# Kernel optimization log

Measured on AMD Instinct MI355X. Metric: run time of the kernel, lower is better.

## Reference

```python
import jax, jax.numpy as jnp
import numpy as np

N_HEAD = 16
N_QUERY_GROUPS = 4
HEAD_SIZE = 64
ROPE_THETA = 10000.0


def apply_rope(x, theta=ROPE_THETA):
    # x: (B, H, T, D) -- lucidrains interleaved-pair rotary embedding
    B, H, T, D = x.shape
    inv_freq = 1.0 / (theta ** (jnp.arange(0, D, 2, dtype=jnp.float32) / D))  # (D/2,)
    freqs = jnp.arange(T, dtype=jnp.float32)[:, None] * inv_freq[None, :]      # (T, D/2)
    freqs = jnp.repeat(freqs, 2, axis=-1)                                      # (T, D)
    cos = jnp.cos(freqs).astype(x.dtype)
    sin = jnp.sin(freqs).astype(x.dtype)
    x1 = x[..., 0::2]
    x2 = x[..., 1::2]
    rot = jnp.stack((-x2, x1), axis=-1).reshape(x.shape)  # rotate_half, interleaved
    return x * cos + rot * sin


def setup_inputs() -> dict:
    key = jax.random.key(0)
    k1, k2, k3 = jax.random.split(key, 3)
    n_embd = N_HEAD * HEAD_SIZE
    qkv_dim = (N_HEAD + 2 * N_QUERY_GROUPS) * HEAD_SIZE
    x = jax.random.normal(k1, (1, 2048, n_embd), dtype=jnp.float32)
    w_attn = jax.random.normal(k2, (n_embd, qkv_dim), dtype=jnp.float32) * (n_embd ** -0.5)
    w_proj = jax.random.normal(k3, (n_embd, n_embd), dtype=jnp.float32) * (n_embd ** -0.5)
    return {"x": x, "w_attn": w_attn, "w_proj": w_proj}


def reference(x, w_attn, w_proj):
    B, T, C = x.shape
    q_per_kv = N_HEAD // N_QUERY_GROUPS
    total_qkv = q_per_kv + 2
    qkv = (x @ w_attn).reshape(B, T, N_QUERY_GROUPS, total_qkv, HEAD_SIZE)
    q = qkv[:, :, :, :q_per_kv, :].reshape(B, T, N_HEAD, HEAD_SIZE)
    k = qkv[:, :, :, q_per_kv:q_per_kv + 1, :].reshape(B, T, N_QUERY_GROUPS, HEAD_SIZE)
    v = qkv[:, :, :, q_per_kv + 1:, :].reshape(B, T, N_QUERY_GROUPS, HEAD_SIZE)
    # (B, H, T, D)
    q = q.transpose(0, 2, 1, 3)
    k = k.transpose(0, 2, 1, 3)
    v = v.transpose(0, 2, 1, 3)
    q = apply_rope(q)
    k = apply_rope(k)
    # GQA: broadcast each kv group to its q_per_kv query heads (repeat_interleave)
    k = jnp.repeat(k, q_per_kv, axis=1)
    v = jnp.repeat(v, q_per_kv, axis=1)
    scale = 1.0 / jnp.sqrt(jnp.asarray(HEAD_SIZE, dtype=q.dtype))
    att = jnp.einsum('bhqd,bhkd->bhqk', q, k) * scale
    causal = jnp.tril(jnp.ones((T, T), dtype=bool))
    att = jnp.where(causal, att, jnp.asarray(-jnp.inf, dtype=att.dtype))
    att = jax.nn.softmax(att, axis=-1)
    y = jnp.einsum('bhqk,bhkd->bhqd', att, v)
    y = y.transpose(0, 2, 1, 3).reshape(B, T, N_HEAD * HEAD_SIZE)
    return y @ w_proj
```

## Files before the change

kernel.cpp:

```cpp
#include <hip/hip_runtime.h>

#define T_SEQ 2048
#define C_EMB 1024
#define C_QKV 1536
#define N_HEAD 16

typedef __bf16 bf16x8 __attribute__((ext_vector_type(8)));
typedef __bf16 bf16x4 __attribute__((ext_vector_type(4)));
typedef float  f32x4  __attribute__((ext_vector_type(4)));

__device__ __forceinline__ void load_lds16(const __bf16* g, __bf16* l)
{
    __builtin_amdgcn_global_load_lds(
        (const __attribute__((address_space(1))) unsigned int*)g,
        (__attribute__((address_space(3))) unsigned int*)l, 16, 0, 0);
}

__device__ __forceinline__ void tconv_tile(
    const float* __restrict__ in, __bf16* __restrict__ out,
    int R, int C, int r0, int c0, float (*lds)[65], int t)
{
#pragma unroll
    for (int k = 0; k < 16; k++) {
        int r = k * 4 + (t >> 6), c = t & 63;
        lds[r][c] = in[(size_t)(r0 + r) * C + c0 + c];
    }
    __syncthreads();
#pragma unroll
    for (int k = 0; k < 16; k++) {
        int cc = k * 4 + (t >> 6), rr = t & 63;
        out[(size_t)(c0 + cc) * R + r0 + rr] = (__bf16)lds[rr][cc];
    }
}

__global__ __launch_bounds__(256) void prep_kernel(
    const float* __restrict__ x, const float* __restrict__ wa,
    const float* __restrict__ wp, __bf16* __restrict__ x_bf,
    __bf16* __restrict__ waT, __bf16* __restrict__ wpT)
{
    __shared__ float lds[64][65];
    const int b = blockIdx.x, t = threadIdx.x;
    if (b < 384) {
        tconv_tile(wa, waT, C_EMB, C_QKV, (b / 24) * 64, (b % 24) * 64, lds, t);
    } else if (b < 640) {
        int b2 = b - 384;
        tconv_tile(wp, wpT, C_EMB, C_EMB, (b2 / 16) * 64, (b2 % 16) * 64, lds, t);
    } else {
        for (int gi = (b - 640) * 256 + t; gi < T_SEQ * C_EMB / 8; gi += 65536) {
            float4 v0 = ((const float4*)x)[gi * 2];
            float4 v1 = ((const float4*)x)[gi * 2 + 1];
            bf16x8 o = { (__bf16)v0.x, (__bf16)v0.y, (__bf16)v0.z, (__bf16)v0.w,
                         (__bf16)v1.x, (__bf16)v1.y, (__bf16)v1.z, (__bf16)v1.w };
            ((bf16x8*)x_bf)[gi] = o;
        }
    }
}

template <bool FUSE_QKV>
__global__ __launch_bounds__(256) void gemm_mfma_kernel(
    const __bf16* __restrict__ A, const __bf16* __restrict__ Bt,
    __bf16* __restrict__ Cq, __bf16* __restrict__ Vt,
    float* __restrict__ Cf, int M, int N, int K)
{
    __shared__ __align__(16) __bf16 As0[64 * 64], As1[64 * 64];
    __shared__ __align__(16) __bf16 Bs0[64 * 64], Bs1[64 * 64];

    const int tid = threadIdx.x;
    const int l = tid & 63, w = tid >> 6;
    const int ln = l & 15, q = l >> 4;
    const int wm = (w & 1) * 32, wn = (w >> 1) * 32;
    const int row0 = blockIdx.y * 64, col0 = blockIdx.x * 64;

    f32x4 acc[2][2];
#pragma unroll
    for (int mi = 0; mi < 2; mi++)
#pragma unroll
        for (int ni = 0; ni < 2; ni++) acc[mi][ni] = (f32x4){0.f, 0.f, 0.f, 0.f};

    auto stage = [&](int k0, __bf16* as, __bf16* bs) {
#pragma unroll
        for (int p = 0; p < 2; p++) {
            int r = p * 32 + w * 8 + (l >> 3);
            int cc = (l & 7) ^ (r & 7);
            load_lds16(A + (size_t)(row0 + r) * K + k0 + cc * 8,
                       as + p * 2048 + w * 512);
            load_lds16(Bt + (size_t)(col0 + r) * K + k0 + cc * 8,
                       bs + p * 2048 + w * 512);
        }
    };
    auto compute = [&](const __bf16* as, const __bf16* bs) {
#pragma unroll
        for (int ki = 0; ki < 2; ki++) {
            bf16x8 af[2], bfr[2];
#pragma unroll
            for (int mi = 0; mi < 2; mi++)
                af[mi] = *(const bf16x8*)&as[(wm + mi * 16 + ln) * 64 +
                                             (((ki * 4 + q) ^ (ln & 7)) * 8)];
#pragma unroll
            for (int ni = 0; ni < 2; ni++)
                bfr[ni] = *(const bf16x8*)&bs[(wn + ni * 16 + ln) * 64 +
                                              (((ki * 4 + q) ^ (ln & 7)) * 8)];
#pragma unroll
            for (int mi = 0; mi < 2; mi++)
#pragma unroll
                for (int ni = 0; ni < 2; ni++)
                    acc[mi][ni] = __builtin_amdgcn_mfma_f32_16x16x32_bf16(
                        af[mi], bfr[ni], acc[mi][ni], 0, 0, 0);
        }
    };

    stage(0, As0, Bs0);
    for (int k0 = 0;; k0 += 128) {
        __syncthreads();
        if (k0 + 64 < K) stage(k0 + 64, As1, Bs1);
        compute(As0, Bs0);
        if (k0 + 64 >= K) break;
        __syncthreads();
        if (k0 + 128 < K) stage(k0 + 128, As0, Bs0);
        compute(As1, Bs1);
        if (k0 + 128 >= K) break;
    }

#pragma unroll
    for (int mi = 0; mi < 2; mi++)
#pragma unroll
        for (int ni = 0; ni < 2; ni++) {
            const int col = col0 + wn + ni * 16 + ln;
            if (!FUSE_QKV) {
#pragma unroll
                for (int reg = 0; reg < 4; reg++) {
                    int row = row0 + wm + mi * 16 + 4 * q + reg;
                    Cf[(size_t)row * N + col] = acc[mi][ni][reg];
                }
            } else {
                const int r = col % 384;
                const int gg = col / 384;
                if (r < 320) {
                    const int d = r & 63;
                    const float inv_freq =
                        __expf(-(float)(d & ~1) * (9.210340371976184f / 64.0f));
                    const float sgn = (d & 1) ? 1.0f : -1.0f;
                    const float osc = (r < 256) ? 0.18033688011112042f : 1.0f;
#pragma unroll
                    for (int reg = 0; reg < 4; reg++) {
                        int row = row0 + wm + mi * 16 + 4 * q + reg;
                        float v = acc[mi][ni][reg];
                        float pv = __shfl_xor(v, 1, 64);
                        float sn, cs;
                        sincosf((float)row * inv_freq, &sn, &cs);
                        Cq[(size_t)row * C_QKV + col] =
                            (__bf16)((v * cs + sgn * pv * sn) * osc);
                    }
                } else {
                    const int d = r - 320;
#pragma unroll
                    for (int reg = 0; reg < 4; reg++) {
                        int row = row0 + wm + mi * 16 + 4 * q + reg;
                        Vt[(size_t)(gg * 64 + d) * T_SEQ + row] =
                            (__bf16)acc[mi][ni][reg];
                    }
                }
            }
        }
}

__global__ __launch_bounds__(256) void attn_mfma_kernel(
    const __bf16* __restrict__ qkv, const __bf16* __restrict__ Vt,
    __bf16* __restrict__ y)
{
    __shared__ __align__(16) __bf16 Ks0[64 * 64], Ks1[64 * 64];
    __shared__ __align__(16) __bf16 Vs0[64 * 64], Vs1[64 * 64];
    __shared__ __align__(16) __bf16 Ps[64 * 72];

    const int tid = threadIdx.x;
    const int l = tid & 63, w = tid >> 6;
    const int ln = l & 15, q = l >> 4;
    const int h = blockIdx.y;
    const int qb = (h & 8) ? (31 - blockIdx.x) : blockIdx.x;
    const int g = h >> 2, hj = h & 3;
    const int qbase = g * 384 + hj * 64;
    const int kbase = g * 384 + 256;

    const int qrow = qb * 64 + w * 16 + ln;
    bf16x8 qa[2];
#pragma unroll
    for (int ki = 0; ki < 2; ki++)
        qa[ki] = *(const bf16x8*)(qkv + (size_t)qrow * C_QKV + qbase +
                                  ki * 32 + q * 8);

    f32x4 O[4];
#pragma unroll
    for (int ni = 0; ni < 4; ni++) O[ni] = (f32x4){0.f, 0.f, 0.f, 0.f};
    float lsum = 0.f;

    auto stage = [&](int kt, __bf16* ks, __bf16* vs) {
#pragma unroll
        for (int p = 0; p < 2; p++) {
            int r = p * 32 + w * 8 + (l >> 3);
            int cc = (l & 7) ^ (r & 7);
            load_lds16(qkv + (size_t)(kt * 64 + r) * C_QKV + kbase + cc * 8,
                       ks + p * 2048 + w * 512);
            load_lds16(Vt + (size_t)(g * 64 + r) * T_SEQ + kt * 64 + cc * 8,
                       vs + p * 2048 + w * 512);
        }
    };
    auto compute = [&](int kt, const __bf16* ks, const __bf16* vs) {
        f32x4 s[4];
#pragma unroll
        for (int ni = 0; ni < 4; ni++) s[ni] = (f32x4){0.f, 0.f, 0.f, 0.f};
#pragma unroll
        for (int ki = 0; ki < 2; ki++)
#pragma unroll
            for (int ni = 0; ni < 4; ni++) {
                bf16x8 kb = *(const bf16x8*)&ks[(ni * 16 + ln) * 64 +
                                                (((ki * 4 + q) ^ (ln & 7)) * 8)];
                s[ni] = __builtin_amdgcn_mfma_f32_16x16x32_bf16(
                    kb, qa[ki], s[ni], 0, 0, 0);
            }

        const bool diag = (kt == qb);
#pragma unroll
        for (int ni = 0; ni < 4; ni++) {
            bf16x4 pp;
#pragma unroll
            for (int reg = 0; reg < 4; reg++) {
                float v = s[ni][reg];
                if (diag && (ni * 16 + 4 * q + reg) > (w * 16 + ln)) v = -1e30f;
                float p = exp2f(v);
                lsum += p;
                pp[reg] = (__bf16)p;
            }
            *(bf16x4*)&Ps[(w * 16 + ln) * 72 + ni * 16 + 4 * q] = pp;
        }

#pragma unroll
        for (int ki = 0; ki < 2; ki++) {
            bf16x8 pa = *(const bf16x8*)&Ps[(w * 16 + ln) * 72 +
                                            ki * 32 + q * 8];
#pragma unroll
            for (int ni = 0; ni < 4; ni++) {
                bf16x8 vb = *(const bf16x8*)&vs[(ni * 16 + ln) * 64 +
                                                (((ki * 4 + q) ^ (ln & 7)) * 8)];
                O[ni] = __builtin_amdgcn_mfma_f32_16x16x32_bf16(
                    vb, pa, O[ni], 0, 0, 0);
            }
        }
    };

    stage(0, Ks0, Vs0);
    for (int kt = 0;; kt += 2) {
        __syncthreads();
        if (kt + 1 <= qb) stage(kt + 1, Ks1, Vs1);
        compute(kt, Ks0, Vs0);
        if (kt + 1 > qb) break;
        __syncthreads();
        if (kt + 2 <= qb) stage(kt + 2, Ks0, Vs0);
        compute(kt + 1, Ks1, Vs1);
        if (kt + 2 > qb) break;
    }

    float ls = lsum;
    ls += __shfl_xor(ls, 16, 64);
    ls += __shfl_xor(ls, 32, 64);
    const float inv = 1.0f / ls;
    const int t = qb * 64 + w * 16 + ln;
#pragma unroll
    for (int ni = 0; ni < 4; ni++) {
        bf16x4 o;
#pragma unroll
        for (int reg = 0; reg < 4; reg++) o[reg] = (__bf16)(O[ni][reg] * inv);
        *(bf16x4*)&y[(size_t)t * C_EMB + h * 64 + ni * 16 + 4 * q] = o;
    }
}

extern "C" void kernel_launch(void* const* d_in, const int* in_sizes, int n_in,
                              void* d_out, int out_size, void* d_ws, size_t ws_size,
                              hipStream_t stream)
{
    const float* x      = (const float*)d_in[0];
    const float* w_attn = (const float*)d_in[1];
    const float* w_proj = (const float*)d_in[2];
    float* out = (float*)d_out;

    __bf16* x_bf = (__bf16*)d_ws;
    __bf16* waT  = x_bf + (size_t)T_SEQ * C_EMB;
    __bf16* wpT  = waT  + (size_t)C_QKV * C_EMB;
    __bf16* qkv  = wpT  + (size_t)C_EMB * C_EMB;
    __bf16* Vt   = qkv  + (size_t)T_SEQ * C_QKV;
    __bf16* y_bf = Vt   + (size_t)256 * T_SEQ;

    prep_kernel<<<896, 256, 0, stream>>>(x, w_attn, w_proj, x_bf, waT, wpT);

    gemm_mfma_kernel<true><<<dim3(C_QKV / 64, T_SEQ / 64), 256, 0, stream>>>(
        x_bf, waT, qkv, Vt, nullptr, T_SEQ, C_QKV, C_EMB);

    attn_mfma_kernel<<<dim3(32, N_HEAD), 256, 0, stream>>>(qkv, Vt, y_bf);

    gemm_mfma_kernel<false><<<dim3(C_EMB / 64, T_SEQ / 64), 256, 0, stream>>>(
        y_bf, wpT, nullptr, nullptr, out, T_SEQ, C_EMB, C_EMB);
}
```

Before: 122.9 us.

## Split long causal attention rows across two blocks and merge partial results

```diff
diff --git a/kernel.cpp b/kernel.cpp
--- a/kernel.cpp
+++ b/kernel.cpp
@@ -166,7 +166,8 @@
 
 __global__ __launch_bounds__(256) void attn_mfma_kernel(
     const __bf16* __restrict__ qkv, const __bf16* __restrict__ Vt,
-    __bf16* __restrict__ y)
+    __bf16* __restrict__ y, __bf16* __restrict__ Opart,
+    float* __restrict__ lpart)
 {
     __shared__ __align__(16) __bf16 Ks0[64 * 64], Ks1[64 * 64];
     __shared__ __align__(16) __bf16 Vs0[64 * 64], Vs1[64 * 64];
@@ -175,8 +176,13 @@
     const int tid = threadIdx.x;
     const int l = tid & 63, w = tid >> 6;
     const int ln = l & 15, q = l >> 4;
-    const int h = blockIdx.y;
-    const int qb = (h & 8) ? (31 - blockIdx.x) : blockIdx.x;
+    const int x = blockIdx.x, h = blockIdx.y;
+    int qb, t0, t1;
+    bool partial;
+    if (x < 16)      { qb = 15 - x;  t0 = 0;             t1 = qb + 1;        partial = false; }
+    else if (x < 32) { qb = x;       t0 = 0;             t1 = (qb + 2) >> 1; partial = true;  }
+    else             { qb = x - 16;  t0 = (qb + 2) >> 1; t1 = qb + 1;        partial = true;  }
+
     const int g = h >> 2, hj = h & 3;
     const int qbase = g * 384 + hj * 64;
     const int kbase = g * 384 + 256;
@@ -247,30 +253,65 @@
         }
     };
 
-    stage(0, Ks0, Vs0);
-    for (int kt = 0;; kt += 2) {
+    stage(t0, Ks0, Vs0);
+    for (int kt = t0;;) {
         __syncthreads();
-        if (kt + 1 <= qb) stage(kt + 1, Ks1, Vs1);
+        if (kt + 1 < t1) stage(kt + 1, Ks1, Vs1);
         compute(kt, Ks0, Vs0);
-        if (kt + 1 > qb) break;
+        if (++kt >= t1) break;
         __syncthreads();
-        if (kt + 2 <= qb) stage(kt + 2, Ks0, Vs0);
-        compute(kt + 1, Ks1, Vs1);
-        if (kt + 2 > qb) break;
+        if (kt + 1 < t1) stage(kt + 1, Ks0, Vs0);
+        compute(kt, Ks1, Vs1);
+        if (++kt >= t1) break;
     }
 
     float ls = lsum;
     ls += __shfl_xor(ls, 16, 64);
     ls += __shfl_xor(ls, 32, 64);
-    const float inv = 1.0f / ls;
     const int t = qb * 64 + w * 16 + ln;
-#pragma unroll
-    for (int ni = 0; ni < 4; ni++) {
-        bf16x4 o;
-#pragma unroll
-        for (int reg = 0; reg < 4; reg++) o[reg] = (__bf16)(O[ni][reg] * inv);
-        *(bf16x4*)&y[(size_t)t * C_EMB + h * 64 + ni * 16 + 4 * q] = o;
-    }
+
+    if (!partial) {
+        const float inv = 1.0f / ls;
+#pragma unroll
+        for (int ni = 0; ni < 4; ni++) {
+            bf16x4 o;
+#pragma unroll
+            for (int reg = 0; reg < 4; reg++) o[reg] = (__bf16)(O[ni][reg] * inv);
+            *(bf16x4*)&y[(size_t)t * C_EMB + h * 64 + ni * 16 + 4 * q] = o;
+        }
+    } else {
+        const int half = (x >= 32);
+        const int tr = t - 1024;
+        __bf16* od = Opart + (size_t)half * 1024 * C_EMB +
+                     (size_t)tr * C_EMB + h * 64;
+        if (q == 0) lpart[half * 16 * 1024 + h * 1024 + tr] = ls;
+#pragma unroll
+        for (int ni = 0; ni < 4; ni++) {
+            bf16x4 o;
+#pragma unroll
+            for (int reg = 0; reg < 4; reg++) o[reg] = (__bf16)O[ni][reg];
+            *(bf16x4*)&od[ni * 16 + 4 * q] = o;
+        }
+    }
+}
+
+__global__ __launch_bounds__(256) void merge_kernel(
+    const __bf16* __restrict__ Opart, const float* __restrict__ lpart,
+    __bf16* __restrict__ y)
+{
+    const size_t base = ((size_t)blockIdx.x * 256 + threadIdx.x) * 8;
+    const int tr = (int)(base >> 10);
+    const int c = (int)(base & 1023);
+    const int h = c >> 6;
+    const float inv = 1.0f / (lpart[h * 1024 + tr] +
+                              lpart[16 * 1024 + h * 1024 + tr]);
+    bf16x8 a = *(const bf16x8*)&Opart[base];
+    bf16x8 b = *(const bf16x8*)&Opart[(size_t)1024 * C_EMB + base];
+    bf16x8 o;
+#pragma unroll
+    for (int i = 0; i < 8; i++)
+        o[i] = (__bf16)(((float)a[i] + (float)b[i]) * inv);
+    *(bf16x8*)&y[(size_t)(1024 + tr) * C_EMB + c] = o;
 }
 
 extern "C" void kernel_launch(void* const* d_in, const int* in_sizes, int n_in,
@@ -288,13 +329,18 @@
     __bf16* qkv  = wpT  + (size_t)C_EMB * C_EMB;
     __bf16* Vt   = qkv  + (size_t)T_SEQ * C_QKV;
     __bf16* y_bf = Vt   + (size_t)256 * T_SEQ;
+    __bf16* Opart = x_bf;
+    float*  lpart = (float*)waT;
 
     prep_kernel<<<896, 256, 0, stream>>>(x, w_attn, w_proj, x_bf, waT, wpT);
 
     gemm_mfma_kernel<true><<<dim3(C_QKV / 64, T_SEQ / 64), 256, 0, stream>>>(
         x_bf, waT, qkv, Vt, nullptr, T_SEQ, C_QKV, C_EMB);
 
-    attn_mfma_kernel<<<dim3(32, N_HEAD), 256, 0, stream>>>(qkv, Vt, y_bf);
+    attn_mfma_kernel<<<dim3(48, N_HEAD), 256, 0, stream>>>(
+        qkv, Vt, y_bf, Opart, lpart);
+
+    merge_kernel<<<512, 256, 0, stream>>>(Opart, lpart, y_bf);
 
     gemm_mfma_kernel<false><<<dim3(C_EMB / 64, T_SEQ / 64), 256, 0, stream>>>(
         y_bf, wpT, nullptr, nullptr, out, T_SEQ, C_EMB, C_EMB);
```

New measurement: 120.0 us. 2.3% less time.
